# Performance work log

Measured on AMD Instinct MI355X. Metric: run time of the kernel, lower is better.

## Reference

```python
import jax, jax.numpy as jnp
import numpy as np
import math

B, C_IN, S, D, H, L, FF = 16, 32, 512, 256, 8, 4, 1024
HD = D // H
EPS = 1e-5


def setup_inputs() -> dict:
    key = jax.random.key(0)
    ks = jax.random.split(key, 32)
    r = lambda k, shp: jax.random.normal(k, shp, dtype=jnp.float32) * 0.02
    inp = {
        'x': jax.random.normal(ks[0], (B, C_IN, S), dtype=jnp.float32),
        'conv1_w': r(ks[1], (D, C_IN, 7)), 'conv1_b': jnp.zeros((D,)),
        'bn1_g': jnp.ones((D,)), 'bn1_b': jnp.zeros((D,)),
        'conv2_w': r(ks[2], (D, D, 5)), 'conv2_b': jnp.zeros((D,)),
        'bn2_g': jnp.ones((D,)), 'bn2_b': jnp.zeros((D,)),
        'ln1_g': jnp.ones((L, D)), 'ln1_b': jnp.zeros((L, D)),
        'wq': r(ks[3], (L, D, D)), 'wk': r(ks[4], (L, D, D)),
        'wv': r(ks[5], (L, D, D)), 'wo': r(ks[6], (L, D, D)),
        'bo': jnp.zeros((L, D)),
        'bias_table': r(ks[7], (L, 2 * S - 1, H)),
        'ln2_g': jnp.ones((L, D)), 'ln2_b': jnp.zeros((L, D)),
        'w1': r(ks[8], (L, D, FF)), 'b1': jnp.zeros((L, FF)),
        'w2': r(ks[9], (L, FF, D)), 'b2': jnp.zeros((L, D)),
        'fn_g': jnp.ones((D,)), 'fn_b': jnp.zeros((D,)),
    }
    return inp


def _conv1d(x, w, b, pad):
    # x: (B, C, T), w: (O, I, K) -> (B, O, T)
    y = jax.lax.conv_general_dilated(x, w, (1,), [(pad, pad)],
                                     dimension_numbers=('NCH', 'OIH', 'NCH'))
    return y + b[None, :, None]


def _bn_eval(x, g, b):
    # eval-mode batchnorm with running mean 0, var 1
    return x * (g / jnp.sqrt(1.0 + EPS))[None, :, None] + b[None, :, None]


def _ln(x, g, b):
    mu = jnp.mean(x, axis=-1, keepdims=True)
    var = jnp.var(x, axis=-1, keepdims=True)
    return (x - mu) / jnp.sqrt(var + EPS) * g + b


def _pos_encoding():
    pos = np.arange(S, dtype=np.float32)[:, None]
    div = np.exp(np.arange(0, D, 2, dtype=np.float32) * (-math.log(10000.0) / D))
    scale = D / S
    pe = np.zeros((S, D), dtype=np.float32)
    pe[:, 0::2] = np.sin(pos * div * scale)
    pe[:, 1::2] = np.cos(pos * div * scale)
    return jnp.asarray(pe)


_REL_IDX = jnp.asarray(np.arange(S)[:, None] - np.arange(S)[None, :] + S - 1)  # (S,S)
_PE = _pos_encoding()


def reference(x, conv1_w, conv1_b, bn1_g, bn1_b, conv2_w, conv2_b, bn2_g, bn2_b,
              ln1_g, ln1_b, wq, wk, wv, wo, bo, bias_table,
              ln2_g, ln2_b, w1, b1, w2, b2, fn_g, fn_b):
    # tokenizer
    h = jax.nn.gelu(_bn_eval(_conv1d(x, conv1_w, conv1_b, 3), bn1_g, bn1_b), approximate=False)
    h = jax.nn.gelu(_bn_eval(_conv1d(h, conv2_w, conv2_b, 2), bn2_g, bn2_b), approximate=False)
    t = jnp.transpose(h, (0, 2, 1))  # (B, S, D)
    # positional encoding
    t = t + _PE[None, :, :]
    scale = HD ** -0.5
    for i in range(L):
        xn = _ln(t, ln1_g[i], ln1_b[i])
        q = (xn @ wq[i]).reshape(B, S, H, HD)
        k = (xn @ wk[i]).reshape(B, S, H, HD)
        v = (xn @ wv[i]).reshape(B, S, H, HD)
        scores = jnp.einsum('bihd,bjhd->bhij', q, k) * scale
        rel = bias_table[i][_REL_IDX]              # (S, S, H)
        scores = scores + jnp.transpose(rel, (2, 0, 1))[None]
        probs = jax.nn.softmax(scores, axis=-1)
        ctx = jnp.einsum('bhij,bjhd->bihd', probs, v).reshape(B, S, D)
        t = t + ctx @ wo[i] + bo[i]
        xn2 = _ln(t, ln2_g[i], ln2_b[i])
        ff = jax.nn.gelu(xn2 @ w1[i] + b1[i], approximate=False) @ w2[i] + b2[i]
        t = t + ff
    return _ln(t, fn_g, fn_b)
```

## Files before the change

### kernel.cpp

```cpp
#include <hip/hip_runtime.h>
#include <hip/hip_bf16.h>
#include <stdint.h>

#define B_   16
#define CIN_ 32
#define S_   512
#define D_   256
#define H_   8
#define L_   4
#define FF_  1024
#define HD_  32
#define EPS_ 1e-5f

typedef __hip_bfloat16 bf16;
typedef __attribute__((ext_vector_type(8))) short short8;
typedef __attribute__((ext_vector_type(4))) float floatx4;

__device__ __forceinline__ float b2f(bf16 v) { return __bfloat162float(v); }
__device__ __forceinline__ bf16 f2b(float v) { return __float2bfloat16(v); }
__device__ __forceinline__ float gelu_f(float v) {
    return 0.5f * v * (1.0f + erff(v * 0.70710678118654752f));
}
__device__ __forceinline__ float pe_val(int s, int d) {
    int m2 = d & ~1;
    float div = expf((float)m2 * (-9.210340371976184f / 256.0f));
    float ang = (float)s * div * 0.5f;
    return (d & 1) ? cosf(ang) : sinf(ang);
}

__device__ __forceinline__ void wtrans_tile(const float* __restrict__ src, bf16* __restrict__ dst,
                                            int K, int N, int n0, int k0, int rowoff,
                                            float (*tile)[33], int tid) {
    int tx = tid & 31, ty0 = tid >> 5;
#pragma unroll
    for (int r = 0; r < 4; ++r) {
        int ky = r * 8 + ty0;
        tile[ky][tx] = src[(long)(k0 + ky) * N + n0 + tx];
    }
    __syncthreads();
#pragma unroll
    for (int r = 0; r < 4; ++r) {
        int ny = r * 8 + ty0;
        dst[(long)(rowoff + n0 + ny) * K + k0 + tx] = f2b(tile[tx][ny]);
    }
}

__global__ void prep_kernel(const float* __restrict__ wq, const float* __restrict__ wk,
                            const float* __restrict__ wv, const float* __restrict__ wo,
                            const float* __restrict__ w1, const float* __restrict__ w2,
                            bf16* __restrict__ wqkvT, bf16* __restrict__ woT,
                            bf16* __restrict__ w1T, bf16* __restrict__ w2T,
                            const float* __restrict__ w1c, const float* __restrict__ cb1,
                            const float* __restrict__ g1, const float* __restrict__ bb1,
                            const float* __restrict__ w2c, const float* __restrict__ cb2,
                            const float* __restrict__ g2, const float* __restrict__ bb2,
                            bf16* __restrict__ c1w, bf16* __restrict__ c2w,
                            float* __restrict__ sh1, float* __restrict__ sh2,
                            float* __restrict__ zpage) {
    __shared__ float tile[32][33];
    int tid = threadIdx.x;
    int bid = blockIdx.x;
    if (bid < 3072) {
        int l = bid / 768, r = bid % 768;
        if (r < 256) {
            int which = r >> 6, rr = r & 63;
            int n0 = (rr & 7) * 32, k0 = (rr >> 3) * 32;
            const float* s = (which == 0 ? wq : which == 1 ? wk : which == 2 ? wv : wo) + (long)l * 65536;
            bf16* d = (which == 3) ? (woT + (long)l * 65536) : (wqkvT + (long)l * 768 * 256);
            wtrans_tile(s, d, 256, 256, n0, k0, (which == 3) ? 0 : which * 256, tile, tid);
        } else if (r < 512) {
            int rr = r - 256;
            int n0 = (rr & 31) * 32, k0 = (rr >> 5) * 32;
            wtrans_tile(w1 + (long)l * 262144, w1T + (long)l * 262144, 256, 1024, n0, k0, 0, tile, tid);
        } else {
            int rr = r - 512;
            int n0 = (rr & 7) * 32, k0 = (rr >> 3) * 32;
            wtrans_tile(w2 + (long)l * 262144, w2T + (long)l * 262144, 1024, 256, n0, k0, 0, tile, tid);
        }
        return;
    }
    int cb = bid - 3072;
    int ty = tid >> 4, t16 = tid & 15;
    float rinv = rsqrtf(1.0f + EPS_);
    if (cb < 16) {
        int o = cb * 16 + ty;
        float scale = g1[o] * rinv;
        if (t16 == 0) sh1[o] = cb1[o] * scale + bb1[o];
        for (int j = t16; j < 256; j += 16) {
            int kk = j >> 5, i = j & 31;
            float v = (kk < 7) ? w1c[o * 224 + i * 7 + kk] * scale : 0.0f;
            c1w[o * 256 + kk * 32 + i] = f2b(v);
        }
    } else if (cb < 32) {
        int o = (cb - 16) * 16 + ty;
        float scale = g2[o] * rinv;
        if (t16 == 0) sh2[o] = cb2[o] * scale + bb2[o];
        for (int j = t16; j < D_ * 5; j += 16) {
            int i = j / 5, kk = j % 5;
            c2w[o * 1280 + kk * 256 + i] = f2b(w2c[o * 1280 + i * 5 + kk] * scale);
        }
    } else {
        if (tid < 64) zpage[tid] = 0.0f;
    }
}

__global__ void im2col1_kernel(const float* __restrict__ x, bf16* __restrict__ col) {
    int kk = blockIdx.x, b = blockIdx.y;
    for (int t = threadIdx.x; t < 512 * 32; t += 256) {
        int s = t & 511, i = t >> 9;
        int sp = s + kk - 3;
        float v = (kk < 7 && sp >= 0 && sp < 512) ? x[((b << 5) + i) * 512 + sp] : 0.0f;
        col[(long)((b << 9) + s) * 256 + kk * 32 + i] = f2b(v);
    }
}

template <bool OUT_BF16>
__global__ void ln_kernel(const float* __restrict__ x, const float* __restrict__ g,
                          const float* __restrict__ bt, float* __restrict__ out_f,
                          bf16* __restrict__ out_b) {
    int row = blockIdx.x;
    int tid = threadIdx.x;
    float v = x[(long)row * D_ + tid];
    float s1 = v, s2 = v * v;
    __shared__ float red[8];
#pragma unroll
    for (int off = 32; off; off >>= 1) {
        s1 += __shfl_xor(s1, off);
        s2 += __shfl_xor(s2, off);
    }
    int wave = tid >> 6;
    if ((tid & 63) == 0) { red[wave] = s1; red[4 + wave] = s2; }
    __syncthreads();
    if (tid == 0) {
        float a = red[0] + red[1] + red[2] + red[3];
        float q = red[4] + red[5] + red[6] + red[7];
        float mu = a * (1.0f / D_);
        float var = q * (1.0f / D_) - mu * mu;
        red[0] = mu;
        red[1] = rsqrtf(var + EPS_);
    }
    __syncthreads();
    float y = (v - red[0]) * red[1] * g[tid] + bt[tid];
    if (OUT_BF16) out_b[(long)row * D_ + tid] = f2b(y);
    else          out_f[(long)row * D_ + tid] = y;
}

template <int ROWS>
__device__ __forceinline__ void stage_sw(const char* gbase, long rs_bytes, int k_byte_off,
                                         char* lds_base, int tid) {
    constexpr int ROUNDS = ROWS / 32;
    char* lp = lds_base + (tid & 192) * 16;
#pragma unroll
    for (int r = 0; r < ROUNDS; ++r) {
        int s = r * 256 + tid;
        int row = s >> 3;
        int q = ((s & 7) ^ (row & 7)) * 16;
        const char* gp = gbase + (long)row * rs_bytes + k_byte_off + q;
        __builtin_amdgcn_global_load_lds((const __attribute__((address_space(1))) void*)gp,
                                         (__attribute__((address_space(3))) void*)(lp + r * 4096),
                                         16, 0, 0);
    }
}
__device__ __forceinline__ int sw_off(int m, int qc) {
    return m * 128 + ((qc ^ (m & 7)) * 16);
}

__device__ __forceinline__ void stage_c2(const char* h1b, int s0, int kt, const char* zp,
                                         char* lds_base, int tid) {
    int kk = kt >> 2;
    int c0 = (kt & 3) * 128;
    char* lp = lds_base + (tid & 192) * 16;
    int row = tid >> 3;
    int q = ((tid & 7) ^ (row & 7)) * 16;
    int sp = s0 + row + kk - 2;
    const char* gp = (sp >= 0 && sp < 512) ? h1b + (long)sp * 512 + c0 + q : zp + q;
    __builtin_amdgcn_global_load_lds((const __attribute__((address_space(1))) void*)gp,
                                     (__attribute__((address_space(3))) void*)lp, 16, 0, 0);
}

enum { FB = 1, FG = 2, FR = 4, FO16 = 8, FPE = 16 };

template <int BM, int NB, int FLAGS, bool VT>
__global__ __launch_bounds__(256) void gemm_sw(const bf16* __restrict__ A, const bf16* __restrict__ Wt,
                                               const float* __restrict__ bias, const float* __restrict__ res,
                                               float* __restrict__ outf, bf16* __restrict__ outb,
                                               bf16* __restrict__ vt, int M, int N, int K) {
    constexpr int FM = BM / 32;
    __shared__ __align__(16) short As[2][BM * 64];
    __shared__ __align__(16) short Bs[2][64 * 64];
    int tid = threadIdx.x;
    int wave = tid >> 6, lane = tid & 63;
    int frow = lane & 15, fquad = lane >> 4;
    int id = blockIdx.x;
    int m_low = id & 7;
    int s = id >> 3;
    int ni = s % NB;
    int mi = (s / NB) * 8 + m_low;
    int m0 = mi * BM, n0 = ni * 64;
    int wm = (wave & 1) * (BM / 2), wn = (wave >> 1) * 32;
    floatx4 acc[FM][2] = {};
    const char* Ab = (const char*)A + (long)m0 * K * 2;
    const char* Bb = (const char*)Wt + (long)n0 * K * 2;
    long rs = (long)K * 2;
    int KT = K >> 6;
    stage_sw<BM>(Ab, rs, 0, (char*)As[0], tid);
    stage_sw<64>(Bb, rs, 0, (char*)Bs[0], tid);
    for (int kt = 0; kt < KT; ++kt) {
        int cur = kt & 1;
        __syncthreads();
        if (kt + 1 < KT) {
            stage_sw<BM>(Ab, rs, (kt + 1) * 128, (char*)As[1 - cur], tid);
            stage_sw<64>(Bb, rs, (kt + 1) * 128, (char*)Bs[1 - cur], tid);
        }
        const char* Ap = (const char*)As[cur];
        const char* Bp = (const char*)Bs[cur];
#pragma unroll
        for (int kh = 0; kh < 2; ++kh) {
            short8 af[FM], bw[2];
#pragma unroll
            for (int i = 0; i < FM; ++i)
                af[i] = *(const short8*)(Ap + sw_off(wm + i * 16 + frow, kh * 4 + fquad));
#pragma unroll
            for (int j = 0; j < 2; ++j)
                bw[j] = *(const short8*)(Bp + sw_off(wn + j * 16 + frow, kh * 4 + fquad));
#pragma unroll
            for (int i = 0; i < FM; ++i)
#pragma unroll
                for (int j = 0; j < 2; ++j)
                    acc[i][j] = __builtin_amdgcn_mfma_f32_16x16x32_bf16(af[i], bw[j], acc[i][j], 0, 0, 0);
        }
    }
#pragma unroll
    for (int i = 0; i < FM; ++i) {
#pragma unroll
        for (int j = 0; j < 2; ++j) {
#pragma unroll
            for (int r = 0; r < 4; ++r) {
                int row = m0 + wm + i * 16 + fquad * 4 + r;
                int col = n0 + wn + j * 16 + frow;
                float v = acc[i][j][r];
                if (FLAGS & FB) v += bias[col];
                if (FLAGS & FG) v = gelu_f(v);
                if (FLAGS & FPE) v += pe_val(row & 511, col);
                if (FLAGS & FR) v += res[(long)row * N + col];
                if (VT) {
                    if (col < 512) {
                        outb[(long)row * 512 + col] = f2b(v);
                    } else {
                        int h = (col - 512) >> 5, d = col & 31;
                        int b = row >> 9, ss = row & 511;
                        vt[(long)((b * 8 + h) * 32 + d) * 512 + ss] = f2b(v);
                    }
                } else if (FLAGS & FO16) {
                    outb[(long)row * N + col] = f2b(v);
                } else {
                    outf[(long)row * N + col] = v;
                }
            }
        }
    }
}

template <int NB>
__global__ __launch_bounds__(256) void gemm_c2(const bf16* __restrict__ h1, const bf16* __restrict__ c2w,
                                               const float* __restrict__ sh2, const float* __restrict__ zp,
                                               float* __restrict__ outf) {
    __shared__ __align__(16) short As[2][32 * 64];
    __shared__ __align__(16) short Bs[2][64 * 64];
    int tid = threadIdx.x;
    int wave = tid >> 6, lane = tid & 63;
    int frow = lane & 15, fquad = lane >> 4;
    int id = blockIdx.x;
    int m_low = id & 7;
    int sdec = id >> 3;
    int ni = sdec % NB;
    int mi = (sdec / NB) * 8 + m_low;
    int m0 = mi * 32, n0 = ni * 64;
    int bb = m0 >> 9, s0 = m0 & 511;
    int wm = (wave & 1) * 16, wn = (wave >> 1) * 32;
    floatx4 acc[2] = {};
    const char* h1b = (const char*)h1 + (long)bb * 512 * 512;
    const char* Bb = (const char*)c2w + (long)n0 * 2560;
    stage_c2(h1b, s0, 0, (const char*)zp, (char*)As[0], tid);
    stage_sw<64>(Bb, 2560, 0, (char*)Bs[0], tid);
    for (int kt = 0; kt < 20; ++kt) {
        int cur = kt & 1;
        __syncthreads();
        if (kt + 1 < 20) {
            stage_c2(h1b, s0, kt + 1, (const char*)zp, (char*)As[1 - cur], tid);
            stage_sw<64>(Bb, 2560, (kt + 1) * 128, (char*)Bs[1 - cur], tid);
        }
        const char* Ap = (const char*)As[cur];
        const char* Bp = (const char*)Bs[cur];
#pragma unroll
        for (int kh = 0; kh < 2; ++kh) {
            short8 af, bw[2];
            af = *(const short8*)(Ap + sw_off(wm + frow, kh * 4 + fquad));
#pragma unroll
            for (int j = 0; j < 2; ++j)
                bw[j] = *(const short8*)(Bp + sw_off(wn + j * 16 + frow, kh * 4 + fquad));
#pragma unroll
            for (int j = 0; j < 2; ++j)
                acc[j] = __builtin_amdgcn_mfma_f32_16x16x32_bf16(af, bw[j], acc[j], 0, 0, 0);
        }
    }
#pragma unroll
    for (int j = 0; j < 2; ++j) {
#pragma unroll
        for (int r = 0; r < 4; ++r) {
            int row = m0 + wm + fquad * 4 + r;
            int col = n0 + wn + j * 16 + frow;
            float v = gelu_f(acc[j][r] + sh2[col]);
            outf[(long)row * 256 + col] = v + pe_val(row & 511, col);
        }
    }
}

#define PSTR2 72
__device__ __forceinline__ void stage_k(const char* gK, int j0, char* dst, int tid) {
    char* lp = dst + (tid & 192) * 16;
#pragma unroll
    for (int r = 0; r < 2; ++r) {
        int l = r * 256 + tid;
        int sr = l >> 3, cp = l & 7;
        int c = cp ^ (sr & 7);
        int j = sr * 2 + (c >> 2), cj = c & 3;
        const char* gp = gK + (long)(j0 + j) * 1024 + cj * 16;
        __builtin_amdgcn_global_load_lds((const __attribute__((address_space(1))) void*)gp,
                                         (__attribute__((address_space(3))) void*)(lp + r * 4096), 16, 0, 0);
    }
}
__device__ __forceinline__ void stage_v(const char* gV, int j0, char* dst, int tid) {
    char* lp = dst + (tid & 192) * 16;
#pragma unroll
    for (int r = 0; r < 2; ++r) {
        int l = r * 256 + tid;
        int row = l >> 4, cp = l & 15;
        int c = cp ^ (row & 7);
        const char* gp = gV + (long)row * 1024 + j0 * 2 + c * 16;
        __builtin_amdgcn_global_load_lds((const __attribute__((address_space(1))) void*)gp,
                                         (__attribute__((address_space(3))) void*)(lp + r * 4096), 16, 0, 0);
    }
}

__global__ __launch_bounds__(256) void fattn_kernel(const bf16* __restrict__ qk,
                                                    const bf16* __restrict__ Vt,
                                                    const float* __restrict__ bias_l,
                                                    bf16* __restrict__ ctx) {
    __shared__ __align__(16) char Ks[2][8192];
    __shared__ __align__(16) char Vs[2][8192];
    __shared__ __align__(16) short Ps[4 * 32 * PSTR2];
    __shared__ float bias_s[640];
    int tid = threadIdx.x;
    int wave = tid >> 6, lane = tid & 63;
    int frow = lane & 15, fquad = lane >> 4;
    int bh = blockIdx.y;
    int b = bh >> 3, h = bh & 7;
    int i0 = blockIdx.x * 128;
    int wm = wave * 32;
    const float scale = 0.17677669529663687f;

    for (int t = tid; t < 639; t += 256) bias_s[t] = bias_l[(i0 + t) * 8 + h];

    short8 qf[2];
#pragma unroll
    for (int i = 0; i < 2; ++i)
        qf[i] = *(const short8*)((const short*)qk +
                 (long)((b << 9) + i0 + wm + i * 16 + frow) * 512 + h * 32 + fquad * 8);

    const char* gK = (const char*)qk + (long)b * 512 * 1024 + 512 + h * 64;
    const char* gV = (const char*)Vt + (long)bh * 32 * 1024;

    floatx4 acc_o[2][2] = {};
    float run_m[2][4], run_l[2][4];
#pragma unroll
    for (int i = 0; i < 2; ++i)
#pragma unroll
        for (int r = 0; r < 4; ++r) { run_m[i][r] = -1e30f; run_l[i][r] = 0.0f; }

    short* Pw = Ps + wave * 32 * PSTR2;
    bf16* Pb = (bf16*)Pw;

    stage_k(gK, 0, Ks[0], tid);
    stage_v(gV, 0, Vs[0], tid);
    for (int tt = 0; tt < 4; ++tt) {
        int cur = tt & 1;
        int j0 = tt * 128;
        __syncthreads();
        if (tt + 1 < 4) {
            stage_k(gK, j0 + 128, Ks[1 - cur], tid);
            stage_v(gV, j0 + 128, Vs[1 - cur], tid);
        }
        const char* Kp = Ks[cur];
        const char* Vp = Vs[cur];

        floatx4 accs[2][8] = {};
#pragma unroll
        for (int jt = 0; jt < 8; ++jt) {
            int j = jt * 16 + frow;
            int sr = j >> 1;
            int c = ((j & 1) << 2) | fquad;
            short8 bk = *(const short8*)(Kp + sr * 128 + (c ^ (sr & 7)) * 16);
#pragma unroll
            for (int i = 0; i < 2; ++i)
                accs[i][jt] = __builtin_amdgcn_mfma_f32_16x16x32_bf16(qf[i], bk, accs[i][jt], 0, 0, 0);
        }
#pragma unroll
        for (int i = 0; i < 2; ++i) {
            int irel = wm + i * 16 + fquad * 4;
#pragma unroll
            for (int jt = 0; jt < 8; ++jt) {
                int jl = j0 + jt * 16 + frow;
#pragma unroll
                for (int r = 0; r < 4; ++r)
                    accs[i][jt][r] = accs[i][jt][r] * scale + bias_s[irel + r + 511 - jl];
            }
        }
#pragma unroll
        for (int i = 0; i < 2; ++i) {
#pragma unroll
            for (int r = 0; r < 4; ++r) {
                float m = -1e30f;
#pragma unroll
                for (int jt = 0; jt < 8; ++jt) m = fmaxf(m, accs[i][jt][r]);
                m = fmaxf(m, __shfl_xor(m, 1));
                m = fmaxf(m, __shfl_xor(m, 2));
                m = fmaxf(m, __shfl_xor(m, 4));
                m = fmaxf(m, __shfl_xor(m, 8));
                float nm = fmaxf(run_m[i][r], m);
                float al = __expf(run_m[i][r] - nm);
                run_m[i][r] = nm;
                float ts = 0.0f;
#pragma unroll
                for (int jt = 0; jt < 8; ++jt) {
                    float p = __expf(accs[i][jt][r] - nm);
                    accs[i][jt][r] = p;
                    ts += p;
                }
                ts += __shfl_xor(ts, 1);
                ts += __shfl_xor(ts, 2);
                ts += __shfl_xor(ts, 4);
                ts += __shfl_xor(ts, 8);
                run_l[i][r] = run_l[i][r] * al + ts;
                acc_o[i][0][r] *= al;
                acc_o[i][1][r] *= al;
            }
        }
#pragma unroll
        for (int ss = 0; ss < 2; ++ss) {
#pragma unroll
            for (int i = 0; i < 2; ++i)
#pragma unroll
                for (int j2 = 0; j2 < 4; ++j2)
#pragma unroll
                    for (int r = 0; r < 4; ++r)
                        Pb[(i * 16 + fquad * 4 + r) * PSTR2 + j2 * 16 + frow] =
                            f2b(accs[i][ss * 4 + j2][r]);
#pragma unroll
            for (int ksub = 0; ksub < 2; ++ksub) {
                short8 ap[2], bv[2];
#pragma unroll
                for (int i = 0; i < 2; ++i)
                    ap[i] = *(const short8*)(Pw + (i * 16 + frow) * PSTR2 + ksub * 32 + fquad * 8);
#pragma unroll
                for (int dt = 0; dt < 2; ++dt) {
                    int row = dt * 16 + frow;
                    int c = ss * 8 + ksub * 4 + fquad;
                    bv[dt] = *(const short8*)(Vp + row * 256 + (c ^ (row & 7)) * 16);
                }
#pragma unroll
                for (int i = 0; i < 2; ++i)
#pragma unroll
                    for (int dt = 0; dt < 2; ++dt)
                        acc_o[i][dt] = __builtin_amdgcn_mfma_f32_16x16x32_bf16(ap[i], bv[dt], acc_o[i][dt], 0, 0, 0);
            }
        }
    }

#pragma unroll
    for (int i = 0; i < 2; ++i) {
#pragma unroll
        for (int r = 0; r < 4; ++r) {
            float inv = 1.0f / run_l[i][r];
            int row = i0 + wm + i * 16 + fquad * 4 + r;
#pragma unroll
            for (int dt = 0; dt < 2; ++dt) {
                int d = dt * 16 + frow;
                ctx[(long)((b << 9) + row) * 256 + h * 32 + d] = f2b(acc_o[i][dt][r] * inv);
            }
        }
    }
}

extern "C" void kernel_launch(void* const* d_in, const int* in_sizes, int n_in,
                              void* d_out, int out_size, void* d_ws, size_t ws_size,
                              hipStream_t stream) {
    const float* x        = (const float*)d_in[0];
    const float* conv1_w  = (const float*)d_in[1];
    const float* conv1_b  = (const float*)d_in[2];
    const float* bn1_g    = (const float*)d_in[3];
    const float* bn1_b    = (const float*)d_in[4];
    const float* conv2_w  = (const float*)d_in[5];
    const float* conv2_b  = (const float*)d_in[6];
    const float* bn2_g    = (const float*)d_in[7];
    const float* bn2_b    = (const float*)d_in[8];
    const float* ln1_g    = (const float*)d_in[9];
    const float* ln1_b    = (const float*)d_in[10];
    const float* wq       = (const float*)d_in[11];
    const float* wk       = (const float*)d_in[12];
    const float* wv       = (const float*)d_in[13];
    const float* wo       = (const float*)d_in[14];
    const float* bo       = (const float*)d_in[15];
    const float* bias_tab = (const float*)d_in[16];
    const float* ln2_g    = (const float*)d_in[17];
    const float* ln2_b    = (const float*)d_in[18];
    const float* w1       = (const float*)d_in[19];
    const float* b1       = (const float*)d_in[20];
    const float* w2       = (const float*)d_in[21];
    const float* b2       = (const float*)d_in[22];
    const float* fn_g     = (const float*)d_in[23];
    const float* fn_b     = (const float*)d_in[24];
    (void)in_sizes; (void)n_in; (void)out_size; (void)ws_size;

    const int M = B_ * S_;
    char* wsb = (char*)d_ws;
    float* t    = (float*)wsb;
    bf16* qk    = (bf16*)(wsb + (8u << 20));
    bf16* h1    = (bf16*)(wsb + (8u << 20));
    char* reg2  = wsb + (16u << 20);
    bf16* Vt    = (bf16*)reg2;
    bf16* ff1   = (bf16*)reg2;
    bf16* col1  = (bf16*)reg2;
    bf16* xnctx = (bf16*)(reg2 + (20u << 20));
    bf16* wqkvT = (bf16*)(wsb + (40u << 20));
    bf16* woT   = wqkvT + (long)L_ * 768 * 256;
    bf16* w1T   = woT + (long)L_ * 256 * 256;
    bf16* w2T   = w1T + (long)L_ * 1024 * 256;
    bf16* c1w   = w2T + (long)L_ * 256 * 1024;
    bf16* c2w   = c1w + 256 * 256;
    float* sh1  = (float*)(c2w + 256 * 1280);
    float* sh2  = sh1 + 256;
    float* zp   = sh2 + 256;

    prep_kernel<<<3105, 256, 0, stream>>>(wq, wk, wv, wo, w1, w2,
                                          wqkvT, woT, w1T, w2T,
                                          conv1_w, conv1_b, bn1_g, bn1_b,
                                          conv2_w, conv2_b, bn2_g, bn2_b,
                                          c1w, c2w, sh1, sh2, zp);

    im2col1_kernel<<<dim3(8, B_), 256, 0, stream>>>(x, col1);
    gemm_sw<32, 4, FB | FG | FO16, false><<<1024, 256, 0, stream>>>(
        col1, c1w, sh1, nullptr, nullptr, h1, nullptr, M, 256, 256);
    gemm_c2<4><<<1024, 256, 0, stream>>>(h1, c2w, sh2, zp, t);

    for (int l = 0; l < L_; ++l) {
        ln_kernel<true><<<M, 256, 0, stream>>>(t, ln1_g + l * D_, ln1_b + l * D_, nullptr, xnctx);
        gemm_sw<64, 12, FO16, true><<<1536, 256, 0, stream>>>(
            xnctx, wqkvT + (long)l * 768 * 256, nullptr, nullptr, nullptr, qk, Vt, M, 768, 256);
        fattn_kernel<<<dim3(4, B_ * H_), 256, 0, stream>>>(
            qk, Vt, bias_tab + (long)l * (2 * S_ - 1) * H_, xnctx);
        gemm_sw<32, 4, FB | FR, false><<<1024, 256, 0, stream>>>(
            xnctx, woT + (long)l * 65536, bo + l * D_, t, t, nullptr, nullptr, M, 256, 256);
        ln_kernel<true><<<M, 256, 0, stream>>>(t, ln2_g + l * D_, ln2_b + l * D_, nullptr, xnctx);
        gemm_sw<64, 16, FB | FG | FO16, false><<<2048, 256, 0, stream>>>(
            xnctx, w1T + (long)l * 262144, b1 + l * FF_, nullptr, nullptr, ff1, nullptr, M, 1024, 256);
        gemm_sw<32, 4, FB | FR, false><<<1024, 256, 0, stream>>>(
            ff1, w2T + (long)l * 262144, b2 + l * D_, t, t, nullptr, nullptr, M, 256, 1024);
    }
    ln_kernel<false><<<M, 256, 0, stream>>>(t, fn_g, fn_b, (float*)d_out, nullptr);
}
```

Before: 538.2 us.

## Fold LayerNorm into following GEMMs via precomputed gamma-weighted columns and row stats

Removes the standalone LayerNorm kernels before the QKV and FF1 GEMMs. LN gamma is folded into the transposed weights, and per-column sums of gamma*W and beta*W are precomputed in the prep kernel. Each GEMM computes per-row mean and variance from the bf16 residual tiles already in LDS and applies the correction in the epilogue. The producing GEMMs also write a bf16 copy of the residual. This saves two launches and a full read/write pass per layer, but the LN statistics now come from bf16-rounded inputs, and an un-normalized activation goes through bf16 before subtracting the mean, which may cost accuracy.

```diff
diff --git a/kernel.cpp b/kernel.cpp
--- a/kernel.cpp
+++ b/kernel.cpp
@@ -27,9 +27,13 @@
     float ang = (float)s * div * 0.5f;
     return (d & 1) ? cosf(ang) : sinf(ang);
 }
+__device__ __forceinline__ float us2f(unsigned short u) {
+    return __uint_as_float(((unsigned)u) << 16);
+}
 
 __device__ __forceinline__ void wtrans_tile(const float* __restrict__ src, bf16* __restrict__ dst,
                                             int K, int N, int n0, int k0, int rowoff,
+                                            const float* __restrict__ gvec,
                                             float (*tile)[33], int tid) {
     int tx = tid & 31, ty0 = tid >> 5;
 #pragma unroll
@@ -38,16 +42,19 @@
         tile[ky][tx] = src[(long)(k0 + ky) * N + n0 + tx];
     }
     __syncthreads();
+    float gs = gvec ? gvec[k0 + tx] : 1.0f;
 #pragma unroll
     for (int r = 0; r < 4; ++r) {
         int ny = r * 8 + ty0;
-        dst[(long)(rowoff + n0 + ny) * K + k0 + tx] = f2b(tile[tx][ny]);
+        dst[(long)(rowoff + n0 + ny) * K + k0 + tx] = f2b(tile[tx][ny] * gs);
     }
 }
 
 __global__ void prep_kernel(const float* __restrict__ wq, const float* __restrict__ wk,
                             const float* __restrict__ wv, const float* __restrict__ wo,
                             const float* __restrict__ w1, const float* __restrict__ w2,
+                            const float* __restrict__ ln1_g, const float* __restrict__ ln1_b,
+                            const float* __restrict__ ln2_g, const float* __restrict__ ln2_b,
                             bf16* __restrict__ wqkvT, bf16* __restrict__ woT,
                             bf16* __restrict__ w1T, bf16* __restrict__ w2T,
                             const float* __restrict__ w1c, const float* __restrict__ cb1,
@@ -56,7 +63,9 @@
                             const float* __restrict__ g2, const float* __restrict__ bb2,
                             bf16* __restrict__ c1w, bf16* __restrict__ c2w,
                             float* __restrict__ sh1, float* __restrict__ sh2,
-                            float* __restrict__ zpage) {
+                            float* __restrict__ zpage,
+                            float* __restrict__ gWq, float* __restrict__ bWq,
+                            float* __restrict__ gWf, float* __restrict__ bWf) {
     __shared__ float tile[32][33];
     int tid = threadIdx.x;
     int bid = blockIdx.x;
@@ -67,15 +76,50 @@
             int n0 = (rr & 7) * 32, k0 = (rr >> 3) * 32;
             const float* s = (which == 0 ? wq : which == 1 ? wk : which == 2 ? wv : wo) + (long)l * 65536;
             bf16* d = (which == 3) ? (woT + (long)l * 65536) : (wqkvT + (long)l * 768 * 256);
-            wtrans_tile(s, d, 256, 256, n0, k0, (which == 3) ? 0 : which * 256, tile, tid);
+            const float* gv = (which == 3) ? nullptr : (ln1_g + l * 256);
+            wtrans_tile(s, d, 256, 256, n0, k0, (which == 3) ? 0 : which * 256, gv, tile, tid);
         } else if (r < 512) {
             int rr = r - 256;
             int n0 = (rr & 31) * 32, k0 = (rr >> 5) * 32;
-            wtrans_tile(w1 + (long)l * 262144, w1T + (long)l * 262144, 256, 1024, n0, k0, 0, tile, tid);
+            wtrans_tile(w1 + (long)l * 262144, w1T + (long)l * 262144, 256, 1024, n0, k0, 0,
+                        ln2_g + l * 256, tile, tid);
         } else {
             int rr = r - 512;
             int n0 = (rr & 7) * 32, k0 = (rr >> 3) * 32;
-            wtrans_tile(w2 + (long)l * 262144, w2T + (long)l * 262144, 1024, 256, n0, k0, 0, tile, tid);
+            wtrans_tile(w2 + (long)l * 262144, w2T + (long)l * 262144, 1024, 256, n0, k0, 0,
+                        nullptr, tile, tid);
+        }
+        return;
+    }
+    if (bid >= 3105) {
+        int j = bid - 3105;
+        int l = j / 7, r = j % 7;
+        int n = tid;
+        if (r < 3) {
+            const float* W = (r == 0 ? wq : r == 1 ? wk : wv) + (long)l * 65536;
+            const float* g = ln1_g + l * 256;
+            const float* bb = ln1_b + l * 256;
+            float sg = 0.0f, sb = 0.0f;
+            for (int k = 0; k < 256; ++k) {
+                float w = W[k * 256 + n];
+                sg += g[k] * w;
+                sb += bb[k] * w;
+            }
+            gWq[l * 768 + r * 256 + n] = sg;
+            bWq[l * 768 + r * 256 + n] = sb;
+        } else {
+            int c = r - 3;
+            const float* W = w1 + (long)l * 262144;
+            const float* g = ln2_g + l * 256;
+            const float* bb = ln2_b + l * 256;
+            float sg = 0.0f, sb = 0.0f;
+            for (int k = 0; k < 256; ++k) {
+                float w = W[k * 1024 + c * 256 + n];
+                sg += g[k] * w;
+                sb += bb[k] * w;
+            }
+            gWf[l * 1024 + c * 256 + n] = sg;
+            bWf[l * 1024 + c * 256 + n] = sb;
         }
         return;
     }
@@ -114,10 +158,8 @@
     }
 }
 
-template <bool OUT_BF16>
 __global__ void ln_kernel(const float* __restrict__ x, const float* __restrict__ g,
-                          const float* __restrict__ bt, float* __restrict__ out_f,
-                          bf16* __restrict__ out_b) {
+                          const float* __restrict__ bt, float* __restrict__ out_f) {
     int row = blockIdx.x;
     int tid = threadIdx.x;
     float v = x[(long)row * D_ + tid];
@@ -140,9 +182,7 @@
         red[1] = rsqrtf(var + EPS_);
     }
     __syncthreads();
-    float y = (v - red[0]) * red[1] * g[tid] + bt[tid];
-    if (OUT_BF16) out_b[(long)row * D_ + tid] = f2b(y);
-    else          out_f[(long)row * D_ + tid] = y;
+    out_f[(long)row * D_ + tid] = (v - red[0]) * red[1] * g[tid] + bt[tid];
 }
 
 template <int ROWS>
@@ -178,16 +218,19 @@
                                      (__attribute__((address_space(3))) void*)lp, 16, 0, 0);
 }
 
-enum { FB = 1, FG = 2, FR = 4, FO16 = 8, FPE = 16 };
+enum { FB = 1, FG = 2, FR = 4, FO16 = 8, FLN = 16, FW16 = 32 };
 
 template <int BM, int NB, int FLAGS, bool VT>
 __global__ __launch_bounds__(256) void gemm_sw(const bf16* __restrict__ A, const bf16* __restrict__ Wt,
                                                const float* __restrict__ bias, const float* __restrict__ res,
+                                               const float* __restrict__ gW, const float* __restrict__ bW,
                                                float* __restrict__ outf, bf16* __restrict__ outb,
-                                               bf16* __restrict__ vt, int M, int N, int K) {
+                                               bf16* __restrict__ out16, bf16* __restrict__ vt,
+                                               int M, int N, int K) {
     constexpr int FM = BM / 32;
     __shared__ __align__(16) short As[2][BM * 64];
     __shared__ __align__(16) short Bs[2][64 * 64];
+    __shared__ float mus[64], rstds[64];
     int tid = threadIdx.x;
     int wave = tid >> 6, lane = tid & 63;
     int frow = lane & 15, fquad = lane >> 4;
@@ -203,6 +246,8 @@
     const char* Bb = (const char*)Wt + (long)n0 * K * 2;
     long rs = (long)K * 2;
     int KT = K >> 6;
+    float s1 = 0.0f, s2 = 0.0f;
+    int srow = tid >> 2, spart = tid & 3;
     stage_sw<BM>(Ab, rs, 0, (char*)As[0], tid);
     stage_sw<64>(Bb, rs, 0, (char*)Bs[0], tid);
     for (int kt = 0; kt < KT; ++kt) {
@@ -214,6 +259,18 @@
         }
         const char* Ap = (const char*)As[cur];
         const char* Bp = (const char*)Bs[cur];
+        if (FLAGS & FLN) {
+#pragma unroll
+            for (int c = 0; c < 2; ++c) {
+                short8 v8 = *(const short8*)(Ap + sw_off(srow, spart * 2 + c));
+#pragma unroll
+                for (int e = 0; e < 8; ++e) {
+                    float f = us2f((unsigned short)v8[e]);
+                    s1 += f;
+                    s2 += f * f;
+                }
+            }
+        }
 #pragma unroll
         for (int kh = 0; kh < 2; ++kh) {
             short8 af[FM], bw[2];
@@ -230,18 +287,33 @@
                     acc[i][j] = __builtin_amdgcn_mfma_f32_16x16x32_bf16(af[i], bw[j], acc[i][j], 0, 0, 0);
         }
     }
+    if (FLAGS & FLN) {
+        s1 += __shfl_xor(s1, 1); s1 += __shfl_xor(s1, 2);
+        s2 += __shfl_xor(s2, 1); s2 += __shfl_xor(s2, 2);
+        if (spart == 0) {
+            float mu = s1 * (1.0f / 256.0f);
+            float var = s2 * (1.0f / 256.0f) - mu * mu;
+            mus[srow] = mu;
+            rstds[srow] = rsqrtf(var + EPS_);
+        }
+        __syncthreads();
+    }
 #pragma unroll
     for (int i = 0; i < FM; ++i) {
 #pragma unroll
         for (int j = 0; j < 2; ++j) {
 #pragma unroll
             for (int r = 0; r < 4; ++r) {
-                int row = m0 + wm + i * 16 + fquad * 4 + r;
+                int rl = wm + i * 16 + fquad * 4 + r;
+                int row = m0 + rl;
                 int col = n0 + wn + j * 16 + frow;
                 float v = acc[i][j][r];
+                if (FLAGS & FLN) {
+                    float rsd = rstds[rl], mm = mus[rl];
+                    v = v * rsd - rsd * mm * gW[col] + bW[col];
+                }
                 if (FLAGS & FB) v += bias[col];
                 if (FLAGS & FG) v = gelu_f(v);
-                if (FLAGS & FPE) v += pe_val(row & 511, col);
                 if (FLAGS & FR) v += res[(long)row * N + col];
                 if (VT) {
                     if (col < 512) {
@@ -256,6 +328,7 @@
                 } else {
                     outf[(long)row * N + col] = v;
                 }
+                if (FLAGS & FW16) out16[(long)row * N + col] = f2b(v);
             }
         }
     }
@@ -264,7 +337,7 @@
 template <int NB>
 __global__ __launch_bounds__(256) void gemm_c2(const bf16* __restrict__ h1, const bf16* __restrict__ c2w,
                                                const float* __restrict__ sh2, const float* __restrict__ zp,
-                                               float* __restrict__ outf) {
+                                               float* __restrict__ outf, bf16* __restrict__ out16) {
     __shared__ __align__(16) short As[2][32 * 64];
     __shared__ __align__(16) short Bs[2][64 * 64];
     int tid = threadIdx.x;
@@ -310,8 +383,9 @@
         for (int r = 0; r < 4; ++r) {
             int row = m0 + wm + fquad * 4 + r;
             int col = n0 + wn + j * 16 + frow;
-            float v = gelu_f(acc[j][r] + sh2[col]);
-            outf[(long)row * 256 + col] = v + pe_val(row & 511, col);
+            float v = gelu_f(acc[j][r] + sh2[col]) + pe_val(row & 511, col);
+            outf[(long)row * 256 + col] = v;
+            out16[(long)row * 256 + col] = f2b(v);
         }
     }
 }
@@ -531,8 +605,9 @@
     bf16* Vt    = (bf16*)reg2;
     bf16* ff1   = (bf16*)reg2;
     bf16* col1  = (bf16*)reg2;
-    bf16* xnctx = (bf16*)(reg2 + (20u << 20));
-    bf16* wqkvT = (bf16*)(wsb + (40u << 20));
+    bf16* t16   = (bf16*)(wsb + (36u << 20));
+    bf16* ctx   = (bf16*)(wsb + (40u << 20));
+    bf16* wqkvT = (bf16*)(wsb + (44u << 20));
     bf16* woT   = wqkvT + (long)L_ * 768 * 256;
     bf16* w1T   = woT + (long)L_ * 256 * 256;
     bf16* w2T   = w1T + (long)L_ * 1024 * 256;
@@ -541,31 +616,39 @@
     float* sh1  = (float*)(c2w + 256 * 1280);
     float* sh2  = sh1 + 256;
     float* zp   = sh2 + 256;
-
-    prep_kernel<<<3105, 256, 0, stream>>>(wq, wk, wv, wo, w1, w2,
+    float* gWq  = zp + 64;
+    float* bWq  = gWq + L_ * 768;
+    float* gWf  = bWq + L_ * 768;
+    float* bWf  = gWf + L_ * 1024;
+
+    prep_kernel<<<3133, 256, 0, stream>>>(wq, wk, wv, wo, w1, w2,
+                                          ln1_g, ln1_b, ln2_g, ln2_b,
                                           wqkvT, woT, w1T, w2T,
                                           conv1_w, conv1_b, bn1_g, bn1_b,
                                           conv2_w, conv2_b, bn2_g, bn2_b,
-                                          c1w, c2w, sh1, sh2, zp);
+                                          c1w, c2w, sh1, sh2, zp,
+                                          gWq, bWq, gWf, bWf);
 
     im2col1_kernel<<<dim3(8, B_), 256, 0, stream>>>(x, col1);
     gemm_sw<32, 4, FB | FG | FO16, false><<<1024, 256, 0, stream>>>(
-        col1, c1w, sh1, nullptr, nullptr, h1, nullptr, M, 256, 256);
-    gemm_c2<4><<<1024, 256, 0, stream>>>(h1, c2w, sh2, zp, t);
+        col1, c1w, sh1, nullptr, nullptr, nullptr, nullptr, h1, nullptr, nullptr, M, 256, 256);
+    gemm_c2<4><<<1024, 256, 0, stream>>>(h1, c2w, sh2, zp, t, t16);
 
     for (int l = 0; l < L_; ++l) {
-        ln_kernel<true><<<M, 256, 0, stream>>>(t, ln1_g + l * D_, ln1_b + l * D_, nullptr, xnctx);
-        gemm_sw<64, 12, FO16, true><<<1536, 256, 0, stream>>>(
-            xnctx, wqkvT + (long)l * 768 * 256, nullptr, nullptr, nullptr, qk, Vt, M, 768, 256);
+        gemm_sw<64, 12, FLN, true><<<1536, 256, 0, stream>>>(
+            t16, wqkvT + (long)l * 768 * 256, nullptr, nullptr,
+            gWq + l * 768, bWq + l * 768, nullptr, qk, nullptr, Vt, M, 768, 256);
         fattn_kernel<<<dim3(4, B_ * H_), 256, 0, stream>>>(
-            qk, Vt, bias_tab + (long)l * (2 * S_ - 1) * H_, xnctx);
-        gemm_sw<32, 4, FB | FR, false><<<1024, 256, 0, stream>>>(
-            xnctx, woT + (long)l * 65536, bo + l * D_, t, t, nullptr, nullptr, M, 256, 256);
-        ln_kernel<true><<<M, 256, 0, stream>>>(t, ln2_g + l * D_, ln2_b + l * D_, nullptr, xnctx);
-        gemm_sw<64, 16, FB | FG | FO16, false><<<2048, 256, 0, stream>>>(
-            xnctx, w1T + (long)l * 262144, b1 + l * FF_, nullptr, nullptr, ff1, nullptr, M, 1024, 256);
-        gemm_sw<32, 4, FB | FR, false><<<1024, 256, 0, stream>>>(
-            ff1, w2T + (long)l * 262144, b2 + l * D_, t, t, nullptr, nullptr, M, 256, 1024);
-    }
-    ln_kernel<false><<<M, 256, 0, stream>>>(t, fn_g, fn_b, (float*)d_out, nullptr);
-}
+            qk, Vt, bias_tab + (long)l * (2 * S_ - 1) * H_, ctx);
+        gemm_sw<32, 4, FB | FR | FW16, false><<<1024, 256, 0, stream>>>(
+            ctx, woT + (long)l * 65536, bo + l * D_, t, nullptr, nullptr,
+            t, nullptr, t16, nullptr, M, 256, 256);
+        gemm_sw<64, 16, FLN | FB | FG | FO16, false><<<2048, 256, 0, stream>>>(
+            t16, w1T + (long)l * 262144, b1 + l * FF_, nullptr,
+            gWf + l * 1024, bWf + l * 1024, nullptr, ff1, nullptr, nullptr, M, 1024, 256);
+        gemm_sw<32, 4, FB | FR | FW16, false><<<1024, 256, 0, stream>>>(
+            ff1, w2T + (long)l * 262144, b2 + l * D_, t, nullptr, nullptr,
+            t, nullptr, t16, nullptr, M, 256, 1024);
+    }
+    ln_kernel<<<M, 256, 0, stream>>>(t, fn_g, fn_b, (float*)d_out);
+}
```

Result: faster. 499.9 us (-7.1%).
